# Kernel optimization log

Measured on AMD Instinct MI355X. Metric: run time of the kernel, lower is better.

## Reference

```python
import jax, jax.numpy as jnp
import numpy as np
from jax.scipy.special import logsumexp

# ---- static hyperparameters (from init_kwargs) ----
NG, NF, NW = 5, 10, 4
STEP = NG + NF + 1            # 16 signatures per writer mini-batch
T, D_FEAT = 512, 64           # sequence length, embedding dim
N = NW * STEP                 # 64 sequences in the batch
GAMMA = 5.0                   # soft-DTW gamma (bandwidth=0.1 -> int 0 -> no band)
MARGIN, ALPHA, BETA = 1.0, 0.1, 1.0
P_W, R_W = 0.1, 0.1
K_NUM, K_MUL = 5, 2.0
BIG = 1e10                    # stand-in for +inf in the DP boundary


def setup_inputs() -> dict:
    key = jax.random.key(0)
    k1, k2 = jax.random.split(key)
    data = jax.random.normal(k1, (N, T, D_FEAT), dtype=jnp.float32)
    lens = jax.random.randint(k2, (N,), T // 2, T + 1).astype(jnp.int32)
    return {"data": data, "lens": lens}


def _softdtw_batch(A, B, la, lb):
    """Batched soft-DTW (squared-Euclidean cost, softmin with gamma).
    A, B: (P, T, d); la, lb: (P,) int lengths. Returns R[la, lb] per pair.
    Anti-diagonal wavefront scan: diagonal k holds R[i, k-i]."""
    P = A.shape[0]
    a2 = jnp.sum(A * A, -1)
    b2 = jnp.sum(B * B, -1)
    Dm = a2[:, :, None] + b2[:, None, :] - 2.0 * jnp.einsum('ptd,psd->pts', A, B)  # (P,T,T)
    i_idx = jnp.arange(T + 1)
    r0 = jnp.broadcast_to(jnp.where(i_idx == 0, 0.0, BIG), (P, T + 1))  # diag k=0: R[0,0]=0
    r1 = jnp.full((P, T + 1), BIG, dtype=A.dtype)                        # diag k=1: boundary inf

    def shift(x):  # x[i] -> x[i-1], pad row i=0 with BIG
        return jnp.concatenate([jnp.full((P, 1), BIG, x.dtype), x[:, :-1]], axis=1)

    def step(carry, k):
        p2, p1 = carry          # diagonals k-2, k-1, each (P, T+1) indexed by i
        j = k - i_idx
        valid = (i_idx >= 1) & (j >= 1) & (j <= T)
        di = jnp.clip(i_idx - 1, 0, T - 1)
        dj = jnp.clip(j - 1, 0, T - 1)
        cost = Dm[:, di, dj]    # (P, T+1)
        # softmin over (R[i-1,j-1], R[i-1,j], R[i,j-1])
        stack = jnp.stack([shift(p2), shift(p1), p1], 0)
        smin = -GAMMA * logsumexp(-stack / GAMMA, axis=0)
        cur = jnp.where(valid[None, :], cost + smin, BIG)
        return (p1, cur), cur

    ks = jnp.arange(2, 2 * T + 1)
    _, ys = jax.lax.scan(step, (r0, r1), ks)  # (2T-1, P, T+1)
    return ys[la + lb - 2, jnp.arange(P), la]


def _mmd_pair(X, Y):
    """Multi-kernel Gaussian MMD between X, Y: (n, F) each."""
    n = X.shape[0]
    total = jnp.concatenate([X, Y], 0)
    sq = jnp.sum(total * total, -1)
    L2 = sq[:, None] + sq[None, :] - 2.0 * total @ total.T
    m = total.shape[0]
    bw = jnp.sum(L2) / (m * m - m)
    bw = bw / (K_MUL ** (K_NUM // 2))
    bws = bw * (K_MUL ** jnp.arange(K_NUM, dtype=X.dtype))
    K = jnp.sum(jnp.exp(-L2[None, :, :] / bws[:, None, None]), 0)
    return (jnp.mean(K[:n, :n]) + jnp.mean(K[n:, n:])
            - jnp.mean(K[:n, n:]) - jnp.mean(K[n:, :n]))


def _forward(data, lens):
    half = NF // 2
    # all anchor/(positive|negative) pairs across writers, flattened: P = NW*(NG+NF)
    a_idx, b_idx = [], []
    for w in range(NW):
        base = w * STEP
        for j in range(1, STEP):
            a_idx.append(base)
            b_idx.append(base + j)
    a_idx = jnp.array(a_idx)
    b_idx = jnp.array(b_idx)
    la, lb = lens[a_idx], lens[b_idx]
    raw = _softdtw_batch(data[a_idx], data[b_idx], la, lb)
    dist = (raw / (la + lb).astype(data.dtype)).reshape(NW, NG + NF)
    dist_g, dist_n = dist[:, :NG], dist[:, NG:]
    dk = jnp.sqrt(jnp.abs(jnp.mean(dist_g, 1)))       # (NW,)
    dg = dist_g / dk[:, None]
    dn = dist_n / dk[:, None]
    lk_s = jax.nn.relu(dg[:, :, None] + MARGIN - dn[:, None, :half])
    lk_r = jax.nn.relu(dg[:, :, None] + MARGIN - dn[:, None, half:])
    ca = jnp.mean(dg, 1)
    cb = jnp.mean(dn[:, :half], 1)
    intra = jnp.sum(dg - ca[:, None], 1)
    inter = jax.nn.relu(BETA - jnp.abs(ca - cb))
    cnt = jax.lax.stop_gradient(
        (jnp.sum(lk_s > 0, (1, 2)) + jnp.sum(lk_r > 0, (1, 2))).astype(data.dtype))
    lv = (jnp.sum(lk_s, (1, 2)) + jnp.sum(lk_r, (1, 2))) / (cnt + 1.0)
    total_loss = jnp.mean(lv + intra * P_W + inter * R_W)

    # pairwise MMD over writer mini-batches (first 1+NG+half signatures each)
    src, tgt = [], []
    for i in range(NW):
        for j in range(1, NW):
            if i != j:
                src.append(np.arange(STEP * i, STEP * (i + 1) - half))
                tgt.append(np.arange(STEP * j, STEP * (j + 1) - half))
    src = jnp.array(np.stack(src))
    tgt = jnp.array(np.stack(tgt))
    Xs = data[src].reshape(src.shape[0], src.shape[1], -1)  # flatten (T,d) per signature
    Ys = data[tgt].reshape(tgt.shape[0], tgt.shape[1], -1)
    mmds = jax.vmap(_mmd_pair)(Xs, Ys)
    siz = NW * (NW + 1) // 2
    mmds = jnp.concatenate([mmds, jnp.zeros(siz - mmds.shape[0], data.dtype)])
    return total_loss + jnp.max(mmds) * ALPHA


def reference(data, lens):
    return _forward(data, lens)
```

## Files before the change

### kernel.cpp

```cpp
#include <hip/hip_runtime.h>
#include <hip/hip_fp16.h>
#include <type_traits>
#include <cstdint>
#include <cstddef>

#define TT 512
#define DFEAT 64
#define NPAIR 60
#define BIGF 1e10f
#define INV_GLN2 0.28853900817779268f
#define NEG_GLN2 -3.4657359027997265f
#define XBIG (-2.8853900817779268e9f)

struct h4 { __half x, y, z, w; };

__constant__ int d_WI[9] = {0,0,0,1,1,2,2,3,3};
__constant__ int d_WJ[9] = {1,2,3,2,3,1,3,1,2};

#if __has_builtin(__builtin_amdgcn_exp2f)
__device__ __forceinline__ float fexp2(float x) { return __builtin_amdgcn_exp2f(x); }
#else
__device__ __forceinline__ float fexp2(float x) { return __expf(0.6931471805599453f * x); }
#endif
#if __has_builtin(__builtin_amdgcn_logf)
__device__ __forceinline__ float flog2(float x) { return __builtin_amdgcn_logf(x); }
#else
__device__ __forceinline__ float flog2(float x) { return 1.4426950408889634f * __logf(x); }
#endif

template <typename CT>
__global__ __launch_bounds__(256) void cost_kernel(const float* __restrict__ data,
                                                   CT* __restrict__ Dm) {
  const int p = blockIdx.z;
  const int w = p / 15, jb = p % 15 + 1;
  const float* __restrict__ A = data + (size_t)(w * 16) * (TT * DFEAT);
  const float* __restrict__ B = data + (size_t)(w * 16 + jb) * (TT * DFEAT);
  const int i0 = blockIdx.y * 64, j0 = blockIdx.x * 64;
  __shared__ float As[64][65];
  __shared__ float Bs[64][65];
  __shared__ float a2[64], b2[64];
  const int tid = threadIdx.x;
#pragma unroll
  for (int s = 0; s < 4; ++s) {
    const int f = tid + s * 256;
    const int r = f >> 4, c4 = (f & 15) << 2;
    float4 va = *(const float4*)(A + (size_t)(i0 + r) * DFEAT + c4);
    As[r][c4 + 0] = va.x; As[r][c4 + 1] = va.y; As[r][c4 + 2] = va.z; As[r][c4 + 3] = va.w;
    float4 vb = *(const float4*)(B + (size_t)(j0 + r) * DFEAT + c4);
    Bs[r][c4 + 0] = vb.x; Bs[r][c4 + 1] = vb.y; Bs[r][c4 + 2] = vb.z; Bs[r][c4 + 3] = vb.w;
  }
  __syncthreads();
  if (tid < 64) {
    float s = 0.f;
#pragma unroll 8
    for (int k = 0; k < 64; ++k) s += As[tid][k] * As[tid][k];
    a2[tid] = s;
  } else if (tid < 128) {
    const int t = tid - 64;
    float s = 0.f;
#pragma unroll 8
    for (int k = 0; k < 64; ++k) s += Bs[t][k] * Bs[t][k];
    b2[t] = s;
  }
  __syncthreads();
  const int ty = tid >> 4, tx = tid & 15;
  float acc[4][4] = {};
#pragma unroll 4
  for (int k = 0; k < 64; ++k) {
    float av[4], bv[4];
#pragma unroll
    for (int r = 0; r < 4; ++r) av[r] = As[ty * 4 + r][k];
#pragma unroll
    for (int c = 0; c < 4; ++c) bv[c] = Bs[tx * 4 + c][k];
#pragma unroll
    for (int r = 0; r < 4; ++r)
#pragma unroll
      for (int c = 0; c < 4; ++c) acc[r][c] += av[r] * bv[c];
  }
  CT* __restrict__ Dp = Dm + (size_t)p * (TT * TT);
  const int band = (i0 >> 3) + (ty >> 1);
  const int sub = (ty & 1) * 4;
#pragma unroll
  for (int c = 0; c < 4; ++c) {
    const int gj = j0 + tx * 4 + c;
    float o[4];
#pragma unroll
    for (int r = 0; r < 4; ++r)
      o[r] = -(a2[ty * 4 + r] + b2[tx * 4 + c] - 2.f * acc[r][c]) * INV_GLN2;
    if constexpr (std::is_same<CT, float>::value) {
      float4 v; v.x = o[0]; v.y = o[1]; v.z = o[2]; v.w = o[3];
      *(float4*)(Dp + (size_t)band * (TT * 8) + (size_t)gj * 8 + sub) = v;
    } else {
      h4 v; v.x = __float2half(o[0]); v.y = __float2half(o[1]);
      v.z = __float2half(o[2]); v.w = __float2half(o[3]);
      *(h4*)(Dp + (size_t)band * (TT * 8) + (size_t)gj * 8 + sub) = v;
    }
  }
}

__device__ __forceinline__ void load8(const float* __restrict__ base, int cc, float* o) {
  const float4* b4 = (const float4*)(base + (size_t)cc * 8);
  float4 a = b4[0], b = b4[1];
  o[0] = a.x; o[1] = a.y; o[2] = a.z; o[3] = a.w;
  o[4] = b.x; o[5] = b.y; o[6] = b.z; o[7] = b.w;
}
__device__ __forceinline__ void load8(const __half* __restrict__ base, int cc, float* o) {
  float4 v = *(const float4*)(base + (size_t)cc * 8);
  const __half2* h = (const __half2*)&v;
#pragma unroll
  for (int q = 0; q < 4; ++q) {
    o[2 * q] = __low2float(h[q]);
    o[2 * q + 1] = __high2float(h[q]);
  }
}

template <typename CT>
__global__ __launch_bounds__(64) void dp_kernel(const CT* __restrict__ Dm,
                                                const int* __restrict__ lens,
                                                float* __restrict__ raw) {
  const int p = blockIdx.x;
  const int w = p / 15, jb = p % 15 + 1;
  const int la = lens[w * 16];
  const int lb = lens[w * 16 + jb];
  const int t = threadIdx.x;
  const int L = (la - 1) >> 3;
  const int dsel = (la - 1) & 7;
  const int s_end = lb + L;

  const CT* __restrict__ base = Dm + (size_t)p * (TT * TT) + (size_t)t * (TT * 8);

  float Xp[8];
#pragma unroll
  for (int d = 0; d < 8; ++d) Xp[d] = XBIG;
  float upA = (t == 0) ? 0.f : XBIG;
  float upB = XBIG;

  float cc_cur[8], cc_n1[8];
  load8(base, 0, cc_cur);
  load8(base, (t == 0) ? 1 : 0, cc_n1);

  for (int s = 1; s <= s_end; ++s) {
    const int cpf = min(max(s - t + 1, 0), TT - 1);
    float n2[8];
    load8(base, cpf, n2);
    const int c = s - t;
    if (c >= 1 && c <= TT) {
      float carryA = upA;
      float Bv = upB;
#pragma unroll
      for (int d = 0; d < 8; ++d) {
        const float A = carryA, B = Bv, C = Xp[d];
        const float M = fmaxf(fmaxf(A, B), C);
        const float e = fexp2(A - M) + fexp2(B - M) + fexp2(C - M);
        const float X = cc_cur[d] + M + flog2(e);
        carryA = C;
        Bv = X;
        Xp[d] = X;
      }
    }
    const float sh = __shfl_up(Xp[7], 1);
    upA = upB;
    upB = (t == 0) ? XBIG : sh;
#pragma unroll
    for (int d = 0; d < 8; ++d) { cc_cur[d] = cc_n1[d]; cc_n1[d] = n2[d]; }
  }
  if (t == L) {
    float xv = Xp[0];
#pragma unroll
    for (int d = 1; d < 8; ++d)
      if (dsel == d) xv = Xp[d];
    raw[p] = NEG_GLN2 * xv;
  }
}

__global__ __launch_bounds__(256) void gram_kernel(const float* __restrict__ data,
                                                   float* __restrict__ partials) {
  const int c = blockIdx.x;
  __shared__ float X[44][516];
  const int tid = threadIdx.x;
#pragma unroll
  for (int s = 0; s < 22; ++s) {
    const int f = tid + s * 256;
    const int r = f >> 7;
    const int c4 = (f & 127) << 2;
    const int n = (r / 11) * 16 + (r % 11);
    float4 v = *(const float4*)(data + (size_t)n * (TT * DFEAT) + c * 512 + c4);
    X[r][c4 + 0] = v.x; X[r][c4 + 1] = v.y; X[r][c4 + 2] = v.z; X[r][c4 + 3] = v.w;
  }
  __syncthreads();
  for (int e = tid; e < 44 * 44; e += 256) {
    const int ii = e / 44, jj = e % 44;
    const float* xi = &X[ii][0];
    const float* xj = &X[jj][0];
    float acc = 0.f;
#pragma unroll 8
    for (int k = 0; k < 512; k += 4) {
      float4 u = *(const float4*)(xi + k);
      float4 v = *(const float4*)(xj + k);
      acc += u.x * v.x + u.y * v.y + u.z * v.z + u.w * v.w;
    }
    partials[(size_t)c * (44 * 44) + e] = acc;
  }
}

__device__ __forceinline__ float blockReduceSum(float v, float* sred) {
#pragma unroll
  for (int off = 32; off > 0; off >>= 1) v += __shfl_down(v, off);
  const int tid = threadIdx.x;
  if ((tid & 63) == 0) sred[tid >> 6] = v;
  __syncthreads();
  const float r = sred[0] + sred[1] + sred[2] + sred[3];
  __syncthreads();
  return r;
}

__global__ __launch_bounds__(256) void final_kernel(const float* __restrict__ partials,
                                                    const float* __restrict__ raw,
                                                    const int* __restrict__ lens,
                                                    float* __restrict__ out) {
  __shared__ float G[44 * 44];
  __shared__ float sred[4];
  const int tid = threadIdx.x;
  for (int e = tid; e < 44 * 44; e += 256) {
    float s = 0.f;
    for (int cc = 0; cc < 64; ++cc) s += partials[(size_t)cc * (44 * 44) + e];
    G[e] = s;
  }
  __syncthreads();
  float maxm = 0.f;
  for (int pp = 0; pp < 9; ++pp) {
    const int wi = d_WI[pp], wj = d_WJ[pp];
    float part = 0.f;
    for (int e = tid; e < 484; e += 256) {
      const int p = e / 22, q = e % 22;
      const int vp = (p < 11) ? (wi * 11 + p) : (wj * 11 + p - 11);
      const int vq = (q < 11) ? (wi * 11 + q) : (wj * 11 + q - 11);
      part += G[vp * 44 + vp] + G[vq * 44 + vq] - 2.f * G[vp * 44 + vq];
    }
    const float suml2 = blockReduceSum(part, sred);
    const float bw = suml2 / 462.0f * 0.25f;
    float aXX = 0.f, aXY = 0.f, aYX = 0.f, aYY = 0.f;
    for (int e = tid; e < 484; e += 256) {
      const int p = e / 22, q = e % 22;
      const int vp = (p < 11) ? (wi * 11 + p) : (wj * 11 + p - 11);
      const int vq = (q < 11) ? (wi * 11 + q) : (wj * 11 + q - 11);
      const float l2 = G[vp * 44 + vp] + G[vq * 44 + vq] - 2.f * G[vp * 44 + vq];
      float kk = 0.f;
      float inv = 1.0f / bw;
#pragma unroll
      for (int tkr = 0; tkr < 5; ++tkr) { kk += __expf(-l2 * inv); inv *= 0.5f; }
      const bool pl = p < 11, ql = q < 11;
      aXX += (pl && ql) ? kk : 0.f;
      aXY += (pl && !ql) ? kk : 0.f;
      aYX += (!pl && ql) ? kk : 0.f;
      aYY += (!pl && !ql) ? kk : 0.f;
    }
    const float sXX = blockReduceSum(aXX, sred);
    const float sXY = blockReduceSum(aXY, sred);
    const float sYX = blockReduceSum(aYX, sred);
    const float sYY = blockReduceSum(aYY, sred);
    if (tid == 0) {
      const float mmd = (sXX + sYY - sXY - sYX) / 121.f;
      maxm = fmaxf(maxm, mmd);
    }
  }
  if (tid == 0) {
    float total = 0.f;
    for (int w = 0; w < 4; ++w) {
      const int la0 = lens[w * 16];
      float dist[15];
      for (int q = 0; q < 15; ++q) {
        const int lb = lens[w * 16 + q + 1];
        dist[q] = raw[w * 15 + q] / (float)(la0 + lb);
      }
      const float mg = (dist[0] + dist[1] + dist[2] + dist[3] + dist[4]) * 0.2f;
      const float dk = sqrtf(fabsf(mg));
      float dg[5], dn[10];
      for (int q = 0; q < 5; ++q) dg[q] = dist[q] / dk;
      for (int q = 0; q < 10; ++q) dn[q] = dist[5 + q] / dk;
      float lsum = 0.f, cnt = 0.f;
      for (int a = 0; a < 5; ++a)
        for (int b = 0; b < 10; ++b) {
          const float v = dg[a] + 1.0f - dn[b];
          if (v > 0.f) { lsum += v; cnt += 1.f; }
        }
      const float ca = (dg[0] + dg[1] + dg[2] + dg[3] + dg[4]) * 0.2f;
      const float cb = (dn[0] + dn[1] + dn[2] + dn[3] + dn[4]) * 0.2f;
      float intra = 0.f;
      for (int q = 0; q < 5; ++q) intra += dg[q] - ca;
      const float inter = fmaxf(1.0f - fabsf(ca - cb), 0.f);
      total += lsum / (cnt + 1.0f) + 0.1f * intra + 0.1f * inter;
    }
    total *= 0.25f;
    out[0] = total + 0.1f * maxm;
  }
}

extern "C" void kernel_launch(void* const* d_in, const int* in_sizes, int n_in,
                              void* d_out, int out_size, void* d_ws, size_t ws_size,
                              hipStream_t stream) {
  const float* data = (const float*)d_in[0];
  const int* lens = (const int*)d_in[1];
  float* out = (float*)d_out;
  char* ws = (char*)d_ws;

  const size_t DMF = (size_t)NPAIR * TT * TT * sizeof(float);
  const size_t DMH = (size_t)NPAIR * TT * TT * sizeof(__half);
  const size_t RAWB = 1024;
  const size_t PARTB = (size_t)64 * 44 * 44 * sizeof(float);

  if (ws_size >= DMF + RAWB + PARTB) {
    float* Dm = (float*)ws;
    float* raw = (float*)(ws + DMF);
    float* partials = (float*)(ws + DMF + RAWB);
    cost_kernel<float><<<dim3(8, 8, NPAIR), 256, 0, stream>>>(data, Dm);
    dp_kernel<float><<<NPAIR, 64, 0, stream>>>(Dm, lens, raw);
    gram_kernel<<<64, 256, 0, stream>>>(data, partials);
    final_kernel<<<1, 256, 0, stream>>>(partials, raw, lens, out);
  } else {
    __half* Dm = (__half*)ws;
    float* raw = (float*)(ws + DMH);
    float* partials = (float*)(ws + DMH + RAWB);
    cost_kernel<__half><<<dim3(8, 8, NPAIR), 256, 0, stream>>>(data, Dm);
    dp_kernel<__half><<<NPAIR, 64, 0, stream>>>(Dm, lens, raw);
    gram_kernel<<<64, 256, 0, stream>>>(data, partials);
    final_kernel<<<1, 256, 0, stream>>>(partials, raw, lens, out);
  }
}
```

Baseline: 360.4 us.

## Run soft-DTW DP in linear domain with mantissa/exponent pairs and bf16 weights

The cost kernel now stores exp2 of the scaled negative cost as bf16, so the DP multiplies by a weight instead of doing exp/log per cell. Each DP value is kept as a separate mantissa and exponent (frexp/ldexp), which avoids the three exp2 and one log2 per cell in the serial wavefront loop. The cost kernel also moves to 128x128 tiles with 8x8 register blocking, precomputed row norms, XOR-swizzled shared memory, and skips tiles beyond the sequence lengths. The DP loop is unrolled by two with the loads prefetched further ahead. The risk is precision: bf16 weights and exponential rescaling may lose accuracy compared with the fp32 log-domain path.

```diff
diff --git a/kernel.cpp b/kernel.cpp
--- a/kernel.cpp
+++ b/kernel.cpp
@@ -1,18 +1,15 @@
 #include <hip/hip_runtime.h>
-#include <hip/hip_fp16.h>
-#include <type_traits>
 #include <cstdint>
 #include <cstddef>
 
 #define TT 512
 #define DFEAT 64
 #define NPAIR 60
-#define BIGF 1e10f
 #define INV_GLN2 0.28853900817779268f
 #define NEG_GLN2 -3.4657359027997265f
-#define XBIG (-2.8853900817779268e9f)
-
-struct h4 { __half x, y, z, w; };
+#define NEGE (-(1 << 29))
+#define BM 128
+#define BK 64
 
 __constant__ int d_WI[9] = {0,0,0,1,1,2,2,3,3};
 __constant__ int d_WJ[9] = {1,2,3,2,3,1,3,1,2};
@@ -27,95 +24,134 @@
 #else
 __device__ __forceinline__ float flog2(float x) { return 1.4426950408889634f * __logf(x); }
 #endif
-
-template <typename CT>
+#if __has_builtin(__builtin_amdgcn_ldexpf)
+__device__ __forceinline__ float fldexp(float x, int n) { return __builtin_amdgcn_ldexpf(x, n); }
+#else
+__device__ __forceinline__ float fldexp(float x, int n) { return ldexpf(x, n); }
+#endif
+#if __has_builtin(__builtin_amdgcn_frexp_mantf)
+__device__ __forceinline__ float fmant(float x) { return __builtin_amdgcn_frexp_mantf(x); }
+#else
+__device__ __forceinline__ float fmant(float x) { int e; return frexpf(x, &e); }
+#endif
+#if __has_builtin(__builtin_amdgcn_frexp_expf)
+__device__ __forceinline__ int fexpo(float x) { return __builtin_amdgcn_frexp_expf(x); }
+#else
+__device__ __forceinline__ int fexpo(float x) { int e; frexpf(x, &e); return e; }
+#endif
+
+__device__ __forceinline__ unsigned short f2bf(float f) {
+  unsigned u = __float_as_uint(f);
+  unsigned r = (u + 0x7FFFu + ((u >> 16) & 1u)) >> 16;
+  return (unsigned short)r;
+}
+
+__global__ __launch_bounds__(256) void norms_kernel(const float* __restrict__ data,
+                                                    float* __restrict__ norms) {
+  const int g = blockIdx.x * 256 + threadIdx.x;
+  const float* __restrict__ row = data + (size_t)g * DFEAT;
+  float s = 0.f;
+#pragma unroll
+  for (int k = 0; k < DFEAT; k += 4) {
+    float4 v = *(const float4*)(row + k);
+    s += v.x * v.x + v.y * v.y + v.z * v.z + v.w * v.w;
+  }
+  norms[g] = s;
+}
+
 __global__ __launch_bounds__(256) void cost_kernel(const float* __restrict__ data,
-                                                   CT* __restrict__ Dm) {
+                                                   const float* __restrict__ norms,
+                                                   const int* __restrict__ lens,
+                                                   unsigned short* __restrict__ Dm) {
   const int p = blockIdx.z;
   const int w = p / 15, jb = p % 15 + 1;
-  const float* __restrict__ A = data + (size_t)(w * 16) * (TT * DFEAT);
-  const float* __restrict__ B = data + (size_t)(w * 16 + jb) * (TT * DFEAT);
-  const int i0 = blockIdx.y * 64, j0 = blockIdx.x * 64;
-  __shared__ float As[64][65];
-  __shared__ float Bs[64][65];
-  __shared__ float a2[64], b2[64];
+  const int la = lens[w * 16], lb = lens[w * 16 + jb];
+  const int i0 = blockIdx.y * BM, j0 = blockIdx.x * BM;
+  if (i0 >= la || j0 >= lb) return;
+  const int an = w * 16, bn = w * 16 + jb;
+  const float* __restrict__ A = data + (size_t)an * (TT * DFEAT);
+  const float* __restrict__ B = data + (size_t)bn * (TT * DFEAT);
+
+  __shared__ float smem[2 * BK * BM];
+  float* As = smem;
+  float* Bs = smem + BK * BM;
+
   const int tid = threadIdx.x;
 #pragma unroll
-  for (int s = 0; s < 4; ++s) {
-    const int f = tid + s * 256;
-    const int r = f >> 4, c4 = (f & 15) << 2;
-    float4 va = *(const float4*)(A + (size_t)(i0 + r) * DFEAT + c4);
-    As[r][c4 + 0] = va.x; As[r][c4 + 1] = va.y; As[r][c4 + 2] = va.z; As[r][c4 + 3] = va.w;
-    float4 vb = *(const float4*)(B + (size_t)(j0 + r) * DFEAT + c4);
-    Bs[r][c4 + 0] = vb.x; Bs[r][c4 + 1] = vb.y; Bs[r][c4 + 2] = vb.z; Bs[r][c4 + 3] = vb.w;
-  }
-  __syncthreads();
-  if (tid < 64) {
-    float s = 0.f;
-#pragma unroll 8
-    for (int k = 0; k < 64; ++k) s += As[tid][k] * As[tid][k];
-    a2[tid] = s;
-  } else if (tid < 128) {
-    const int t = tid - 64;
-    float s = 0.f;
-#pragma unroll 8
-    for (int k = 0; k < 64; ++k) s += Bs[t][k] * Bs[t][k];
-    b2[t] = s;
-  }
-  __syncthreads();
+  for (int s2 = 0; s2 < 8; ++s2) {
+    const int f = tid + s2 * 256;
+    const int row = f >> 4;
+    const int k4 = (f & 15) << 2;
+    float4 va = *(const float4*)(A + (size_t)(i0 + row) * DFEAT + k4);
+    float4 vb = *(const float4*)(B + (size_t)(j0 + row) * DFEAT + k4);
+#pragma unroll
+    for (int q = 0; q < 4; ++q) {
+      const int k = k4 + q;
+      const int cp = row ^ (k & 24);
+      As[k * BM + cp] = ((const float*)&va)[q];
+      Bs[k * BM + cp] = ((const float*)&vb)[q];
+    }
+  }
   const int ty = tid >> 4, tx = tid & 15;
-  float acc[4][4] = {};
+  const int r0 = ty * 8, c0 = tx * 8;
+  float aI[8], bI[8];
+#pragma unroll
+  for (int q = 0; q < 8; ++q) {
+    aI[q] = norms[(size_t)an * TT + i0 + r0 + q] * INV_GLN2;
+    bI[q] = norms[(size_t)bn * TT + j0 + c0 + q] * INV_GLN2;
+  }
+  __syncthreads();
+
+  float acc[8][8] = {};
 #pragma unroll 4
-  for (int k = 0; k < 64; ++k) {
-    float av[4], bv[4];
-#pragma unroll
-    for (int r = 0; r < 4; ++r) av[r] = As[ty * 4 + r][k];
-#pragma unroll
-    for (int c = 0; c < 4; ++c) bv[c] = Bs[tx * 4 + c][k];
-#pragma unroll
-    for (int r = 0; r < 4; ++r)
-#pragma unroll
-      for (int c = 0; c < 4; ++c) acc[r][c] += av[r] * bv[c];
-  }
-  CT* __restrict__ Dp = Dm + (size_t)p * (TT * TT);
-  const int band = (i0 >> 3) + (ty >> 1);
-  const int sub = (ty & 1) * 4;
-#pragma unroll
-  for (int c = 0; c < 4; ++c) {
-    const int gj = j0 + tx * 4 + c;
-    float o[4];
-#pragma unroll
-    for (int r = 0; r < 4; ++r)
-      o[r] = -(a2[ty * 4 + r] + b2[tx * 4 + c] - 2.f * acc[r][c]) * INV_GLN2;
-    if constexpr (std::is_same<CT, float>::value) {
-      float4 v; v.x = o[0]; v.y = o[1]; v.z = o[2]; v.w = o[3];
-      *(float4*)(Dp + (size_t)band * (TT * 8) + (size_t)gj * 8 + sub) = v;
-    } else {
-      h4 v; v.x = __float2half(o[0]); v.y = __float2half(o[1]);
-      v.z = __float2half(o[2]); v.w = __float2half(o[3]);
-      *(h4*)(Dp + (size_t)band * (TT * 8) + (size_t)gj * 8 + sub) = v;
-    }
-  }
-}
-
-__device__ __forceinline__ void load8(const float* __restrict__ base, int cc, float* o) {
-  const float4* b4 = (const float4*)(base + (size_t)cc * 8);
-  float4 a = b4[0], b = b4[1];
-  o[0] = a.x; o[1] = a.y; o[2] = a.z; o[3] = a.w;
-  o[4] = b.x; o[5] = b.y; o[6] = b.z; o[7] = b.w;
-}
-__device__ __forceinline__ void load8(const __half* __restrict__ base, int cc, float* o) {
-  float4 v = *(const float4*)(base + (size_t)cc * 8);
-  const __half2* h = (const __half2*)&v;
-#pragma unroll
-  for (int q = 0; q < 4; ++q) {
-    o[2 * q] = __low2float(h[q]);
-    o[2 * q + 1] = __high2float(h[q]);
-  }
-}
-
-template <typename CT>
-__global__ __launch_bounds__(64) void dp_kernel(const CT* __restrict__ Dm,
+  for (int k = 0; k < BK; ++k) {
+    const int v = k & 24;
+    float af[8], bf8[8];
+    *(float4*)&af[0] = *(const float4*)&As[k * BM + (r0 ^ v)];
+    *(float4*)&af[4] = *(const float4*)&As[k * BM + (r0 ^ v) + 4];
+    *(float4*)&bf8[0] = *(const float4*)&Bs[k * BM + (c0 ^ v)];
+    *(float4*)&bf8[4] = *(const float4*)&Bs[k * BM + (c0 ^ v) + 4];
+#pragma unroll
+    for (int r = 0; r < 8; ++r)
+#pragma unroll
+      for (int cc = 0; cc < 8; ++cc)
+        acc[r][cc] += af[r] * bf8[cc];
+  }
+  __syncthreads();
+
+  unsigned short* wst = (unsigned short*)smem;
+  const float twoInv = 2.0f * INV_GLN2;
+#pragma unroll
+  for (int cc = 0; cc < 8; ++cc) {
+    const int col = c0 + cc;
+    unsigned short t8[8];
+#pragma unroll
+    for (int r = 0; r < 8; ++r) {
+      const float x = twoInv * acc[r][cc] - aI[r] - bI[cc];
+      t8[r] = f2bf(fexp2(x));
+    }
+    const int G = ty * 128 + col;
+    const int Gs = G ^ (tx & 7);
+    const unsigned u0 = (unsigned)t8[0] | ((unsigned)t8[1] << 16);
+    const unsigned u1 = (unsigned)t8[2] | ((unsigned)t8[3] << 16);
+    const unsigned u2 = (unsigned)t8[4] | ((unsigned)t8[5] << 16);
+    const unsigned u3 = (unsigned)t8[6] | ((unsigned)t8[7] << 16);
+    uint4 vv; vv.x = u0; vv.y = u1; vv.z = u2; vv.w = u3;
+    *(uint4*)&wst[Gs * 8] = vv;
+  }
+  __syncthreads();
+  unsigned short* __restrict__ Dp = Dm + (size_t)p * (TT * TT);
+#pragma unroll
+  for (int s2 = 0; s2 < 8; ++s2) {
+    const int g = tid + s2 * 256;
+    const int band = g >> 7, col = g & 127;
+    const int Gs = g ^ ((col >> 3) & 7);
+    uint4 vv = *(const uint4*)&wst[Gs * 8];
+    *(uint4*)(Dp + (size_t)((i0 >> 3) + band) * (TT * 8) + (size_t)(j0 + col) * 8) = vv;
+  }
+}
+
+__global__ __launch_bounds__(64) void dp_kernel(const unsigned short* __restrict__ Dm,
                                                 const int* __restrict__ lens,
                                                 float* __restrict__ raw) {
   const int p = blockIdx.x;
@@ -127,49 +163,87 @@
   const int dsel = (la - 1) & 7;
   const int s_end = lb + L;
 
-  const CT* __restrict__ base = Dm + (size_t)p * (TT * TT) + (size_t)t * (TT * 8);
-
-  float Xp[8];
-#pragma unroll
-  for (int d = 0; d < 8; ++d) Xp[d] = XBIG;
-  float upA = (t == 0) ? 0.f : XBIG;
-  float upB = XBIG;
-
-  float cc_cur[8], cc_n1[8];
-  load8(base, 0, cc_cur);
-  load8(base, (t == 0) ? 1 : 0, cc_n1);
-
-  for (int s = 1; s <= s_end; ++s) {
-    const int cpf = min(max(s - t + 1, 0), TT - 1);
-    float n2[8];
-    load8(base, cpf, n2);
-    const int c = s - t;
+  const unsigned short* __restrict__ base = Dm + (size_t)p * (TT * TT) + (size_t)t * (TT * 8);
+
+  float Xm[8]; int Xe[8];
+#pragma unroll
+  for (int d = 0; d < 8; ++d) { Xm[d] = 0.f; Xe[d] = NEGE; }
+  float upAm = (t == 0) ? 0.5f : 0.f;
+  int   upAe = (t == 0) ? 1 : NEGE;
+  float upBm = 0.f;
+  int   upBe = NEGE;
+
+  auto colidx = [&](int sigma) { return min(max(sigma - t - 1, 0), TT - 1); };
+  auto ldcol = [&](int cc) { return *(const uint4*)(base + (size_t)cc * 8); };
+
+  float WA[8], WB[8];
+  uint4 q0 = ldcol(colidx(1));
+  uint4 q1 = ldcol(colidx(2));
+  uint4 RA = ldcol(colidx(3));
+  uint4 RB = ldcol(colidx(4));
+  {
+    const unsigned ua[4] = {q0.x, q0.y, q0.z, q0.w};
+    const unsigned ub[4] = {q1.x, q1.y, q1.z, q1.w};
+#pragma unroll
+    for (int i = 0; i < 4; ++i) {
+      WA[2*i]   = __uint_as_float(ua[i] << 16);
+      WA[2*i+1] = __uint_as_float(ua[i] & 0xFFFF0000u);
+      WB[2*i]   = __uint_as_float(ub[i] << 16);
+      WB[2*i+1] = __uint_as_float(ub[i] & 0xFFFF0000u);
+    }
+  }
+
+  auto decode8 = [&](const uint4& q, float* o) {
+    const unsigned u[4] = {q.x, q.y, q.z, q.w};
+#pragma unroll
+    for (int i = 0; i < 4; ++i) {
+      o[2*i]   = __uint_as_float(u[i] << 16);
+      o[2*i+1] = __uint_as_float(u[i] & 0xFFFF0000u);
+    }
+  };
+
+  auto step = [&](int sigma, float* W) {
+    const int c = sigma - t;
     if (c >= 1 && c <= TT) {
-      float carryA = upA;
-      float Bv = upB;
+      float Am = upAm; int Ae = upAe;
+      float Bm = upBm; int Be = upBe;
 #pragma unroll
       for (int d = 0; d < 8; ++d) {
-        const float A = carryA, B = Bv, C = Xp[d];
-        const float M = fmaxf(fmaxf(A, B), C);
-        const float e = fexp2(A - M) + fexp2(B - M) + fexp2(C - M);
-        const float X = cc_cur[d] + M + flog2(e);
-        carryA = C;
-        Bv = X;
-        Xp[d] = X;
+        const float Cm = Xm[d]; const int Ce = Xe[d];
+        const int em = max(max(Ae, Be), Ce);
+        const float sum = fldexp(Am, Ae - em) + fldexp(Cm, Ce - em) + fldexp(Bm, Be - em);
+        const float pr = W[d] * sum;
+        const float nm = fmant(pr);
+        const int ne = em + fexpo(pr);
+        Am = Cm; Ae = Ce;
+        Bm = nm; Be = ne;
+        Xm[d] = nm; Xe[d] = ne;
       }
     }
-    const float sh = __shfl_up(Xp[7], 1);
-    upA = upB;
-    upB = (t == 0) ? XBIG : sh;
-#pragma unroll
-    for (int d = 0; d < 8; ++d) { cc_cur[d] = cc_n1[d]; cc_n1[d] = n2[d]; }
-  }
+    const float shm = __shfl_up(Xm[7], 1);
+    const int she = __shfl_up(Xe[7], 1);
+    upAm = upBm; upAe = upBe;
+    upBm = (t == 0) ? 0.f : shm;
+    upBe = (t == 0) ? NEGE : she;
+  };
+
+  int s = 1;
+  for (; s + 1 <= s_end; s += 2) {
+    step(s, WA);
+    decode8(RA, WA);
+    RA = ldcol(colidx(s + 4));
+    step(s + 1, WB);
+    decode8(RB, WB);
+    RB = ldcol(colidx(s + 5));
+  }
+  if (s <= s_end) step(s, WA);
+
   if (t == L) {
-    float xv = Xp[0];
+    float xm = Xm[0]; int xe = Xe[0];
 #pragma unroll
     for (int d = 1; d < 8; ++d)
-      if (dsel == d) xv = Xp[d];
-    raw[p] = NEG_GLN2 * xv;
+      if (dsel == d) { xm = Xm[d]; xe = Xe[d]; }
+    raw[p] = NEG_GLN2 * ((float)xe + flog2(xm));
   }
 }
 
@@ -304,26 +378,18 @@
   float* out = (float*)d_out;
   char* ws = (char*)d_ws;
 
-  const size_t DMF = (size_t)NPAIR * TT * TT * sizeof(float);
-  const size_t DMH = (size_t)NPAIR * TT * TT * sizeof(__half);
+  const size_t DMB = (size_t)NPAIR * TT * TT * sizeof(unsigned short);
   const size_t RAWB = 1024;
   const size_t PARTB = (size_t)64 * 44 * 44 * sizeof(float);
 
-  if (ws_size >= DMF + RAWB + PARTB) {
-    float* Dm = (float*)ws;
-    float* raw = (float*)(ws + DMF);
-    float* partials = (float*)(ws + DMF + RAWB);
-    cost_kernel<float><<<dim3(8, 8, NPAIR), 256, 0, stream>>>(data, Dm);
-    dp_kernel<float><<<NPAIR, 64, 0, stream>>>(Dm, lens, raw);
-    gram_kernel<<<64, 256, 0, stream>>>(data, partials);
-    final_kernel<<<1, 256, 0, stream>>>(partials, raw, lens, out);
-  } else {
-    __half* Dm = (__half*)ws;
-    float* raw = (float*)(ws + DMH);
-    float* partials = (float*)(ws + DMH + RAWB);
-    cost_kernel<__half><<<dim3(8, 8, NPAIR), 256, 0, stream>>>(data, Dm);
-    dp_kernel<__half><<<NPAIR, 64, 0, stream>>>(Dm, lens, raw);
-    gram_kernel<<<64, 256, 0, stream>>>(data, partials);
-    final_kernel<<<1, 256, 0, stream>>>(partials, raw, lens, out);
-  }
-}
+  unsigned short* Dm = (unsigned short*)ws;
+  float* raw = (float*)(ws + DMB);
+  float* partials = (float*)(ws + DMB + RAWB);
+  float* norms = (float*)(ws + DMB + RAWB + PARTB);
+
+  norms_kernel<<<128, 256, 0, stream>>>(data, norms);
+  cost_kernel<<<dim3(4, 4, NPAIR), 256, 0, stream>>>(data, norms, lens, Dm);
+  dp_kernel<<<NPAIR, 64, 0, stream>>>(Dm, lens, raw);
+  gram_kernel<<<64, 256, 0, stream>>>(data, partials);
+  final_kernel<<<1, 256, 0, stream>>>(partials, raw, lens, out);
+}
```

Measured after the change: 317.4 us. -12.0%, faster.
